# Kernel tuning notes

Hardware: AMD Instinct MI355X
Metric: run time of the kernel (lower is better)

Reference implementation:

```python
import jax, jax.numpy as jnp
import numpy as np
import math

B, T, C = 2, 2048, 1024
H, DK, DV = 16, 64, 64


def setup_inputs() -> dict:
    key = jax.random.key(0)
    ks = jax.random.split(key, 5)
    # randw(*d) = randn(*d) / sqrt(d[-1])
    x = jax.random.normal(ks[0], (B, T, C), dtype=jnp.float32)
    w_q = jax.random.normal(ks[1], (H, DK, C), dtype=jnp.float32) / math.sqrt(C)
    w_k = jax.random.normal(ks[2], (H, DK, C), dtype=jnp.float32) / math.sqrt(C)
    w_v = jax.random.normal(ks[3], (H, DV, C), dtype=jnp.float32) / math.sqrt(C)
    w_o = jax.random.normal(ks[4], (H * DV, C), dtype=jnp.float32) / math.sqrt(C)
    return {"x": x, "w_q": w_q, "w_k": w_k, "w_v": w_v, "w_o": w_o}


def reference(x, w_q, w_k, w_v, w_o):
    # Full prefill: bs_q.first = 0, bs_q.nb = T, causal=True, dropout=0 (eval).
    dk = w_q.shape[1]
    q = jnp.einsum('ntc,hdc->nhtd', x, w_q)  # [B,H,T,DK]
    k = jnp.einsum('ntc,hdc->nhtd', x, w_k)  # [B,H,T,DK]
    v = jnp.einsum('ntc,hdc->nhtd', x, w_v)  # [B,H,T,DV]
    a = jnp.einsum('nhtd,nhsd->nhts', q, k) / jnp.sqrt(jnp.asarray(dk, x.dtype))
    # amm_generator: mask where query_idx < key_idx (strict upper triangle)
    t = a.shape[-1]
    mask = jnp.arange(t)[:, None] < jnp.arange(t)[None, :]  # [T,T] bool
    a = jnp.where(mask[None, None], jnp.asarray(-jnp.inf, a.dtype), a)
    a = jax.nn.softmax(a, axis=-1)
    y = jnp.einsum('nhts,nhsd->nthd', a, v)  # [B,T,H,DV]
    y = y.reshape(y.shape[0], y.shape[1], -1)  # [B,T,H*DV]
    return y @ w_o  # [B,T,C]
```

## Files before the change

### kernel.cpp

```cpp
#include <hip/hip_runtime.h>
#include <hip/hip_bf16.h>

#define B_ 2
#define T_ 2048
#define C_ 1024
#define H_ 16
#define D_ 64

typedef __attribute__((ext_vector_type(8))) short bf16x8;
typedef __attribute__((ext_vector_type(4))) float f32x4;
typedef __attribute__((ext_vector_type(8))) unsigned short u16x8;
typedef __attribute__((ext_vector_type(2))) unsigned int u32x2;
typedef __attribute__((ext_vector_type(4))) unsigned int u32x4;

__device__ __forceinline__ unsigned short bf1(float a) {
    __bf16 x = (__bf16)a;
    return __builtin_bit_cast(unsigned short, x);
}
__device__ __forceinline__ unsigned int pk2(float a, float b) {
    return (unsigned int)bf1(a) | ((unsigned int)bf1(b) << 16);
}
__device__ __forceinline__ float bf2f(unsigned short u) {
    union { unsigned int u; float f; } v; v.u = (unsigned int)u << 16;
    return v.f;
}

__device__ __forceinline__ void gll16(const void* g, void* l) {
    __builtin_amdgcn_global_load_lds(
        (const __attribute__((address_space(1))) unsigned int*)g,
        (__attribute__((address_space(3))) unsigned int*)l, 16, 0, 0);
}

__global__ __launch_bounds__(256) void prep_x(
    const float* __restrict__ x, unsigned short* __restrict__ xb)
{
    const size_t i = ((size_t)blockIdx.x * 256 + threadIdx.x) * 16;
    float4 f0 = *reinterpret_cast<const float4*>(x + i);
    float4 f1 = *reinterpret_cast<const float4*>(x + i + 4);
    float4 f2 = *reinterpret_cast<const float4*>(x + i + 8);
    float4 f3 = *reinterpret_cast<const float4*>(x + i + 12);
    u32x4 a = {pk2(f0.x, f0.y), pk2(f0.z, f0.w), pk2(f1.x, f1.y), pk2(f1.z, f1.w)};
    u32x4 b = {pk2(f2.x, f2.y), pk2(f2.z, f2.w), pk2(f3.x, f3.y), pk2(f3.z, f3.w)};
    *reinterpret_cast<u32x4*>(xb + i) = a;
    *reinterpret_cast<u32x4*>(xb + i + 8) = b;
}

__global__ __launch_bounds__(256) void prep_w(
    const float* __restrict__ wq, const float* __restrict__ wk,
    const float* __restrict__ wv, unsigned short* __restrict__ wb)
{
    const int bid = blockIdx.x, tid = threadIdx.x;
    const int rb = bid * 4;
    const float* src = (rb < 1024) ? wq + (size_t)rb * 1024
                     : (rb < 2048) ? wk + (size_t)(rb - 1024) * 1024
                                   : wv + (size_t)(rb - 2048) * 1024;
    const float sc = (rb < 1024) ? 0.125f * 1.4426950408889634f : 1.0f;
    const float4* s4 = (const float4*)src;
    u32x2* d = (u32x2*)(wb + (size_t)rb * 1024);
#pragma unroll
    for (int k = 0; k < 4; k++) {
        float4 v = s4[k * 256 + tid];
        u32x2 w;
        w[0] = pk2(v.x * sc, v.y * sc);
        w[1] = pk2(v.z * sc, v.w * sc);
        d[k * 256 + tid] = w;
    }
}

__global__ __launch_bounds__(256) void prep_wo(
    const float* __restrict__ wo, unsigned short* __restrict__ wt)
{
    __shared__ unsigned short tile[64][72];
    const int tk = (blockIdx.x & 15) << 6, tn = (blockIdx.x >> 4) << 6;
    const int r = threadIdx.x >> 2, cb = (threadIdx.x & 3) << 4;
#pragma unroll
    for (int j = 0; j < 4; j++) {
        float4 v = *reinterpret_cast<const float4*>(
            wo + (size_t)(tk + r) * 1024 + tn + cb + j * 4);
        u32x2 w;
        w[0] = pk2(v.x, v.y);
        w[1] = pk2(v.z, v.w);
        *reinterpret_cast<u32x2*>(&tile[r][cb + j * 4]) = w;
    }
    __syncthreads();
    unsigned short buf[16];
#pragma unroll
    for (int j = 0; j < 16; j++) buf[j] = tile[cb + j][r];
    unsigned short* dst = wt + (size_t)(tn + r) * 1024 + tk + cb;
    *reinterpret_cast<u16x8*>(dst) = *reinterpret_cast<u16x8*>(buf);
    *reinterpret_cast<u16x8*>(dst + 8) = *reinterpret_cast<u16x8*>(buf + 8);
}

__global__ __launch_bounds__(256) void qkv_gemm(
    const unsigned short* __restrict__ xb, const unsigned short* __restrict__ wb,
    unsigned short* __restrict__ qkv)
{
    __shared__ __align__(16) unsigned short As[128 * 32];
    __shared__ __align__(16) unsigned short Bs[128 * 32];
    const int tid = threadIdx.x;
    const int lane = tid & 63, wave = tid >> 6;
    const int g = lane >> 4, c16 = lane & 15;
    const int xcd = blockIdx.x & 7, idx = blockIdx.x >> 3;
    const int bm = (xcd << 2) + idx / 24, bn = idx % 24;
    const int jbase = bn << 7;
    const int which = jbase >> 10;

    const int srow = lane >> 2, sch = (lane & 3) << 3;
    const unsigned short* asrc = xb + ((size_t)(bm << 7) + wave * 32 + srow) * C_ + sch;
    const unsigned short* bsrc = wb + ((size_t)(bn << 7) + wave * 32 + srow) * C_ + sch;

    f32x4 acc[4][4];
#pragma unroll
    for (int i = 0; i < 4; i++)
#pragma unroll
        for (int j = 0; j < 4; j++) acc[i][j] = (f32x4){0.f, 0.f, 0.f, 0.f};

    const int wm = (wave >> 1) << 6, wn = (wave & 1) << 6;

    for (int t = 0; t < 32; ++t) {
        const int k0 = t << 5;
        __syncthreads();
        gll16(asrc + k0,           &As[(wave * 32) << 5]);
        gll16(asrc + k0 + 16 * C_, &As[(wave * 32 + 16) << 5]);
        gll16(bsrc + k0,           &Bs[(wave * 32) << 5]);
        gll16(bsrc + k0 + 16 * C_, &Bs[(wave * 32 + 16) << 5]);
        __syncthreads();

        bf16x8 af[4], bfv[4];
#pragma unroll
        for (int m = 0; m < 4; m++)
            af[m] = *reinterpret_cast<const bf16x8*>(&As[((wm + m * 16 + c16) << 5) + g * 8]);
#pragma unroll
        for (int n = 0; n < 4; n++)
            bfv[n] = *reinterpret_cast<const bf16x8*>(&Bs[((wn + n * 16 + c16) << 5) + g * 8]);
#pragma unroll
        for (int m = 0; m < 4; m++)
#pragma unroll
            for (int n = 0; n < 4; n++)
                acc[m][n] = __builtin_amdgcn_mfma_f32_16x16x32_bf16(af[m], bfv[n], acc[m][n], 0, 0, 0);
    }

    if (which < 2) {
#pragma unroll
        for (int m = 0; m < 4; m++) {
            const int grow = (bm << 7) + wm + m * 16 + (g << 2);
#pragma unroll
            for (int n = 0; n < 4; n++) {
                const int jj = (jbase + wn + n * 16 + c16) & 1023;
                const int h = jj >> 6, d = jj & 63;
#pragma unroll
                for (int r = 0; r < 4; r++) {
                    const int row = grow + r;
                    const int b = row >> 11, t = row & 2047;
                    const size_t off = ((size_t)((which * B_ + b) * H_ + h) * T_ + t) * 64 + d;
                    qkv[off] = bf1(acc[m][n][r]);
                }
            }
        }
    } else {
#pragma unroll
        for (int m = 0; m < 4; m++) {
            const int grow = (bm << 7) + wm + m * 16 + (g << 2);
            const int b = grow >> 11, t = grow & 2047;
#pragma unroll
            for (int n = 0; n < 4; n++) {
                const int jj = (jbase + wn + n * 16 + c16) & 1023;
                const int h = jj >> 6, d = jj & 63;
                u32x2 w;
                w[0] = pk2(acc[m][n][0], acc[m][n][1]);
                w[1] = pk2(acc[m][n][2], acc[m][n][3]);
                const size_t off = ((size_t)((2 * B_ + b) * H_ + h) * 64 + d) * T_ + t;
                *reinterpret_cast<u32x2*>(&qkv[off]) = w;
            }
        }
    }
}

__global__ __launch_bounds__(256) void attn(
    const unsigned short* __restrict__ qkv,
    unsigned short* __restrict__ opA, unsigned short* __restrict__ opB,
    float* __restrict__ lbuf)
{
    __shared__ __align__(16) unsigned short Ks[2][64 * 64];
    __shared__ __align__(16) unsigned short Vt[2][64 * 64];
    __shared__ __align__(16) unsigned short Ps[4][16 * 64];
    const int tid = threadIdx.x, lane = tid & 63, wave = tid >> 6;
    const int g = lane >> 4, c16 = lane & 15;
    const int qt = 31 - (blockIdx.x >> 6);
    const int rem = blockIdx.x & 63;
    const int half = rem >> 5, bh = rem & 31;
    const int b = bh >> 4, h = bh & 15;
    const size_t headoff = (size_t)(b * H_ + h) * T_ * 64;
    const size_t QSZ = (size_t)B_ * H_ * T_ * 64;
    const unsigned short* qp = qkv + headoff;
    const unsigned short* kp = qkv + QSZ + headoff;
    const unsigned short* vTp = qkv + 2 * QSZ + headoff;

    const int nt = qt + 1;
    const int h1 = (nt + 1) >> 1;
    const int itlo = half ? h1 : 0, ithi = half ? nt : h1;

    const int qbase = (qt << 6) + wave * 16;
    bf16x8 qf0, qf1;
    {
        const size_t r0 = (size_t)(qbase + c16) * 64;
        qf0 = *reinterpret_cast<const bf16x8*>(qp + r0 + g * 8);
        qf1 = *reinterpret_cast<const bf16x8*>(qp + r0 + 32 + g * 8);
    }

    const bf16x8 ones = {0x3F80, 0x3F80, 0x3F80, 0x3F80, 0x3F80, 0x3F80, 0x3F80, 0x3F80};
    f32x4 lacc = (f32x4){0.f, 0.f, 0.f, 0.f};
    f32x4 acc[4];
#pragma unroll
    for (int i = 0; i < 4; i++) acc[i] = (f32x4){0.f, 0.f, 0.f, 0.f};

    const int srow8 = lane >> 3;
    const int swc = ((lane & 7) ^ srow8) << 3;
    const unsigned short* ksrc = kp + (size_t)(wave * 16 + srow8) * 64 + swc;
    const unsigned short* vsrc = vTp + (size_t)(wave * 16 + srow8) * T_ + swc;

    auto stage = [&](int buf, int s0) {
#pragma unroll
        for (int i = 0; i < 2; i++) {
            gll16(ksrc + (size_t)(s0 + i * 8) * 64, &Ks[buf][(wave * 16 + i * 8) << 6]);
            gll16(vsrc + s0 + (size_t)i * 8 * T_, &Vt[buf][(wave * 16 + i * 8) << 6]);
        }
    };

    if (itlo < ithi) {
        stage(0, itlo << 6);
        int cur = 0;
        for (int it = itlo; it < ithi; ++it) {
            __syncthreads();
            if (it + 1 < ithi) stage(cur ^ 1, (it + 1) << 6);
            const int s0 = it << 6;

            f32x4 sfT[4];
#pragma unroll
            for (int f = 0; f < 4; f++) sfT[f] = (f32x4){-16.f, -16.f, -16.f, -16.f};
            __builtin_amdgcn_s_setprio(1);
#pragma unroll
            for (int f = 0; f < 4; f++) {
                const int row = f * 16 + c16;
                const int sw = row & 7;
                bf16x8 k0 = *reinterpret_cast<const bf16x8*>(&Ks[cur][(row << 6) + ((g ^ sw) << 3)]);
                bf16x8 k1 = *reinterpret_cast<const bf16x8*>(&Ks[cur][(row << 6) + (((g + 4) ^ sw) << 3)]);
                sfT[f] = __builtin_amdgcn_mfma_f32_16x16x32_bf16(k0, qf0, sfT[f], 0, 0, 0);
                sfT[f] = __builtin_amdgcn_mfma_f32_16x16x32_bf16(k1, qf1, sfT[f], 0, 0, 0);
            }
            __builtin_amdgcn_s_setprio(0);

            if (it == qt) {
                const int qglob = qbase + c16;
#pragma unroll
                for (int f = 0; f < 4; f++)
#pragma unroll
                    for (int r = 0; r < 4; r++) {
                        const int kv = s0 + f * 16 + g * 4 + r;
                        if (kv > qglob) sfT[f][r] = -1e30f;
                    }
            }

#pragma unroll
            for (int f = 0; f < 4; f++)
#pragma unroll
                for (int r = 0; r < 4; r++)
                    sfT[f][r] = __builtin_amdgcn_exp2f(sfT[f][r]);

#pragma unroll
            for (int f = 0; f < 4; f++) {
                u32x2 w;
                w[0] = pk2(sfT[f][0], sfT[f][1]);
                w[1] = pk2(sfT[f][2], sfT[f][3]);
                const int addr = (c16 << 6) + ((((f << 1) + (g >> 1)) ^ (c16 & 7)) << 3) + ((g & 1) << 2);
                *reinterpret_cast<u32x2*>(&Ps[wave][addr]) = w;
            }

            __builtin_amdgcn_s_setprio(1);
#pragma unroll
            for (int ks = 0; ks < 2; ks++) {
                bf16x8 pa = *reinterpret_cast<const bf16x8*>(
                    &Ps[wave][(c16 << 6) + ((((ks << 2) + g) ^ (c16 & 7)) << 3)]);
                lacc = __builtin_amdgcn_mfma_f32_16x16x32_bf16(ones, pa, lacc, 0, 0, 0);
#pragma unroll
                for (int fd = 0; fd < 4; fd++) {
                    const int d = fd * 16 + c16;
                    bf16x8 vf = *reinterpret_cast<const bf16x8*>(
                        &Vt[cur][(d << 6) + ((((ks << 2) + g) ^ (d & 7)) << 3)]);
                    acc[fd] = __builtin_amdgcn_mfma_f32_16x16x32_bf16(vf, pa, acc[fd], 0, 0, 0);
                }
            }
            __builtin_amdgcn_s_setprio(0);
            cur ^= 1;
        }
    }

    unsigned short* op = half ? opB : opA;
#pragma unroll
    for (int fd = 0; fd < 4; fd++) {
        u32x2 w;
        w[0] = pk2(acc[fd][0], acc[fd][1]);
        w[1] = pk2(acc[fd][2], acc[fd][3]);
        const size_t cy = ((size_t)b * T_ + qbase + c16) * 1024 + h * 64 + fd * 16 + g * 4;
        *reinterpret_cast<u32x2*>(&op[cy]) = w;
    }
    if (lane < 16)
        lbuf[(size_t)half * (B_ * H_ * T_) + ((size_t)(b * H_ + h)) * T_ + qbase + c16] = lacc[0];
}

__global__ __launch_bounds__(256) void combine(
    const unsigned short* __restrict__ opA, const unsigned short* __restrict__ opB,
    const float* __restrict__ lbuf, unsigned short* __restrict__ y)
{
    const size_t i = ((size_t)blockIdx.x * 256 + threadIdx.x) * 8;
    const int hh = (int)((i >> 6) & 15);
    const int t = (int)((i >> 10) & 2047);
    const int bb = (int)(i >> 21);
    const size_t li = ((size_t)(bb * H_ + hh)) * T_ + t;
    const float inv = 1.0f / (lbuf[li] + lbuf[(size_t)B_ * H_ * T_ + li]);
    u16x8 a = *reinterpret_cast<const u16x8*>(opA + i);
    u16x8 c = *reinterpret_cast<const u16x8*>(opB + i);
    unsigned short o[8];
#pragma unroll
    for (int j = 0; j < 8; j++) o[j] = bf1((bf2f(a[j]) + bf2f(c[j])) * inv);
    *reinterpret_cast<u16x8*>(y + i) = *reinterpret_cast<u16x8*>(o);
}

__global__ __launch_bounds__(256) void out_proj(
    const unsigned short* __restrict__ y, const unsigned short* __restrict__ wt,
    float* __restrict__ out)
{
    __shared__ __align__(16) unsigned short As[128 * 32];
    __shared__ __align__(16) unsigned short Bs[64 * 32];
    const int tid = threadIdx.x;
    const int lane = tid & 63, wave = tid >> 6;
    const int g = lane >> 4, c16 = lane & 15;
    const int xcd = blockIdx.x & 7, idx = blockIdx.x >> 3;
    const int bm = (xcd << 2) + (idx >> 4), bn = idx & 15;
    const int wm = (wave >> 1) << 6, wn = (wave & 1) << 5;

    const int srow = lane >> 2, sch = (lane & 3) << 3;
    const unsigned short* ysrc = y + ((size_t)(bm << 7) + wave * 32 + srow) * 1024 + sch;
    const unsigned short* wsrc = wt + ((size_t)(bn << 6) + wave * 16 + srow) * 1024 + sch;

    f32x4 acc[4][2];
#pragma unroll
    for (int i = 0; i < 4; i++)
#pragma unroll
        for (int j = 0; j < 2; j++) acc[i][j] = (f32x4){0.f, 0.f, 0.f, 0.f};

    for (int t = 0; t < 32; ++t) {
        const int k0 = t << 5;
        __syncthreads();
        gll16(ysrc + k0,            &As[(wave * 32) << 5]);
        gll16(ysrc + k0 + 16 * 1024, &As[(wave * 32 + 16) << 5]);
        gll16(wsrc + k0,            &Bs[(wave * 16) << 5]);
        __syncthreads();

        bf16x8 af[4], bfr[2];
#pragma unroll
        for (int m = 0; m < 4; m++)
            af[m] = *reinterpret_cast<const bf16x8*>(&As[((wm + m * 16 + c16) << 5) + g * 8]);
#pragma unroll
        for (int n = 0; n < 2; n++)
            bfr[n] = *reinterpret_cast<const bf16x8*>(&Bs[((wn + n * 16 + c16) << 5) + g * 8]);
#pragma unroll
        for (int m = 0; m < 4; m++)
#pragma unroll
            for (int n = 0; n < 2; n++)
                acc[m][n] = __builtin_amdgcn_mfma_f32_16x16x32_bf16(af[m], bfr[n], acc[m][n], 0, 0, 0);
    }

#pragma unroll
    for (int m = 0; m < 4; m++) {
        const int grow = (bm << 7) + wm + m * 16 + (g << 2);
#pragma unroll
        for (int n = 0; n < 2; n++) {
            const int gcol = (bn << 6) + wn + n * 16 + c16;
#pragma unroll
            for (int r = 0; r < 4; r++)
                out[(size_t)(grow + r) * 1024 + gcol] = acc[m][n][r];
        }
    }
}

extern "C" void kernel_launch(void* const* d_in, const int* in_sizes, int n_in,
                              void* d_out, int out_size, void* d_ws, size_t ws_size,
                              hipStream_t stream) {
    const float* x  = (const float*)d_in[0];
    const float* wq = (const float*)d_in[1];
    const float* wk = (const float*)d_in[2];
    const float* wv = (const float*)d_in[3];
    const float* wo = (const float*)d_in[4];
    float* out = (float*)d_out;

    unsigned short* wb   = (unsigned short*)d_ws;
    unsigned short* opB  = (unsigned short*)d_ws;
    unsigned short* y    = opB;
    unsigned short* qkv  = (unsigned short*)d_ws + (size_t)4 * 1024 * 1024;
    unsigned short* wt   = qkv;
    unsigned short* xb   = (unsigned short*)d_out;
    unsigned short* opA  = (unsigned short*)d_out;
    float* lbuf = (float*)((char*)d_out + (size_t)8 * 1024 * 1024);

    prep_x<<<dim3(1024), 256, 0, stream>>>(x, xb);
    prep_w<<<dim3(768), 256, 0, stream>>>(wq, wk, wv, wb);
    qkv_gemm<<<dim3(768), 256, 0, stream>>>(xb, wb, qkv);
    attn<<<dim3(2048), 256, 0, stream>>>(qkv, opA, opB, lbuf);
    combine<<<dim3(4096), 256, 0, stream>>>(opA, opB, lbuf, y);
    prep_wo<<<dim3(256), 256, 0, stream>>>(wo, wt);
    out_proj<<<dim3(512), 256, 0, stream>>>(y, wt, out);
}
```

Measured before the change: 116.8 us.

## Process two query tiles per attention block to reuse staged K/V

Each attention block now handles 128 query rows (two 64-row tiles per wave set) instead of 64, so every K/V tile staged into shared memory feeds twice as many MFMAs. The KV range is split into two halves aligned to the 128-row tile, and the double-buffered loop is manually unrolled by two with precomputed swizzled LDS pointers. A fully masked first sub-tile skips its exp and PV work. This halves the grid and the global K/V traffic per query row, at the cost of more registers and fewer blocks to balance the causal workload.

New measurement: 116.7 us. Within noise of the previous version (-0.1%).

```diff
diff --git a/kernel.cpp b/kernel.cpp
--- a/kernel.cpp
+++ b/kernel.cpp
@@ -181,14 +181,14 @@
     unsigned short* __restrict__ opA, unsigned short* __restrict__ opB,
     float* __restrict__ lbuf)
 {
-    __shared__ __align__(16) unsigned short Ks[2][64 * 64];
-    __shared__ __align__(16) unsigned short Vt[2][64 * 64];
+    __shared__ __align__(16) unsigned short Ks0[64 * 64], Ks1[64 * 64];
+    __shared__ __align__(16) unsigned short Vt0[64 * 64], Vt1[64 * 64];
     __shared__ __align__(16) unsigned short Ps[4][16 * 64];
     const int tid = threadIdx.x, lane = tid & 63, wave = tid >> 6;
     const int g = lane >> 4, c16 = lane & 15;
-    const int qt = 31 - (blockIdx.x >> 6);
+    const int qt = 15 - (blockIdx.x >> 6);
     const int rem = blockIdx.x & 63;
-    const int half = rem >> 5, bh = rem & 31;
+    const int split = rem >> 5, bh = rem & 31;
     const int b = bh >> 4, h = bh & 15;
     const size_t headoff = (size_t)(b * H_ + h) * T_ * 64;
     const size_t QSZ = (size_t)B_ * H_ * T_ * 64;
@@ -196,116 +196,192 @@
     const unsigned short* kp = qkv + QSZ + headoff;
     const unsigned short* vTp = qkv + 2 * QSZ + headoff;
 
-    const int nt = qt + 1;
-    const int h1 = (nt + 1) >> 1;
-    const int itlo = half ? h1 : 0, ithi = half ? nt : h1;
-
-    const int qbase = (qt << 6) + wave * 16;
-    bf16x8 qf0, qf1;
+    const int h1 = qt + 1;
+    const int itlo = split ? h1 : 0, ithi = split ? (2 * qt + 2) : h1;
+
+    const int qb0 = (qt << 7) + wave * 16;
+    const int qb1 = qb0 + 64;
+    bf16x8 qf00, qf01, qf10, qf11;
     {
-        const size_t r0 = (size_t)(qbase + c16) * 64;
-        qf0 = *reinterpret_cast<const bf16x8*>(qp + r0 + g * 8);
-        qf1 = *reinterpret_cast<const bf16x8*>(qp + r0 + 32 + g * 8);
+        const size_t r0 = (size_t)(qb0 + c16) * 64;
+        const size_t r1 = (size_t)(qb1 + c16) * 64;
+        qf00 = *reinterpret_cast<const bf16x8*>(qp + r0 + g * 8);
+        qf01 = *reinterpret_cast<const bf16x8*>(qp + r0 + 32 + g * 8);
+        qf10 = *reinterpret_cast<const bf16x8*>(qp + r1 + g * 8);
+        qf11 = *reinterpret_cast<const bf16x8*>(qp + r1 + 32 + g * 8);
     }
 
     const bf16x8 ones = {0x3F80, 0x3F80, 0x3F80, 0x3F80, 0x3F80, 0x3F80, 0x3F80, 0x3F80};
-    f32x4 lacc = (f32x4){0.f, 0.f, 0.f, 0.f};
-    f32x4 acc[4];
-#pragma unroll
-    for (int i = 0; i < 4; i++) acc[i] = (f32x4){0.f, 0.f, 0.f, 0.f};
+    f32x4 lac0 = (f32x4){0.f, 0.f, 0.f, 0.f}, lac1 = (f32x4){0.f, 0.f, 0.f, 0.f};
+    f32x4 acc0[4], acc1[4];
+#pragma unroll
+    for (int i = 0; i < 4; i++) {
+        acc0[i] = (f32x4){0.f, 0.f, 0.f, 0.f};
+        acc1[i] = (f32x4){0.f, 0.f, 0.f, 0.f};
+    }
+
+    const int sw = c16 & 7;
+    const int rdo0 = (c16 << 6) + ((g ^ sw) << 3);
+    const int rdo1 = (c16 << 6) + (((g + 4) ^ sw) << 3);
+    const unsigned short* krA0 = Ks0 + rdo0;
+    const unsigned short* krA1 = Ks0 + rdo1;
+    const unsigned short* krB0 = Ks1 + rdo0;
+    const unsigned short* krB1 = Ks1 + rdo1;
+    const unsigned short* vrA0 = Vt0 + rdo0;
+    const unsigned short* vrA1 = Vt0 + rdo1;
+    const unsigned short* vrB0 = Vt1 + rdo0;
+    const unsigned short* vrB1 = Vt1 + rdo1;
+    const unsigned short* par0 = Ps[wave] + rdo0;
+    const unsigned short* par1 = Ps[wave] + rdo1;
+    unsigned short* pw[4];
+#pragma unroll
+    for (int f = 0; f < 4; f++)
+        pw[f] = Ps[wave] + (c16 << 6)
+              + (((((f << 1) + (g >> 1))) ^ sw) << 3) + ((g & 1) << 2);
 
     const int srow8 = lane >> 3;
     const int swc = ((lane & 7) ^ srow8) << 3;
     const unsigned short* ksrc = kp + (size_t)(wave * 16 + srow8) * 64 + swc;
     const unsigned short* vsrc = vTp + (size_t)(wave * 16 + srow8) * T_ + swc;
 
-    auto stage = [&](int buf, int s0) {
+    auto stageTo = [&](unsigned short* kd, unsigned short* vd, int s0) {
 #pragma unroll
         for (int i = 0; i < 2; i++) {
-            gll16(ksrc + (size_t)(s0 + i * 8) * 64, &Ks[buf][(wave * 16 + i * 8) << 6]);
-            gll16(vsrc + s0 + (size_t)i * 8 * T_, &Vt[buf][(wave * 16 + i * 8) << 6]);
+            gll16(ksrc + (size_t)(s0 + i * 8) * 64, kd + ((wave * 16 + i * 8) << 6));
+            gll16(vsrc + s0 + (size_t)i * 8 * T_, vd + ((wave * 16 + i * 8) << 6));
         }
     };
 
-    if (itlo < ithi) {
-        stage(0, itlo << 6);
-        int cur = 0;
-        for (int it = itlo; it < ithi; ++it) {
-            __syncthreads();
-            if (it + 1 < ithi) stage(cur ^ 1, (it + 1) << 6);
-            const int s0 = it << 6;
-
-            f32x4 sfT[4];
-#pragma unroll
-            for (int f = 0; f < 4; f++) sfT[f] = (f32x4){-16.f, -16.f, -16.f, -16.f};
-            __builtin_amdgcn_s_setprio(1);
-#pragma unroll
-            for (int f = 0; f < 4; f++) {
-                const int row = f * 16 + c16;
-                const int sw = row & 7;
-                bf16x8 k0 = *reinterpret_cast<const bf16x8*>(&Ks[cur][(row << 6) + ((g ^ sw) << 3)]);
-                bf16x8 k1 = *reinterpret_cast<const bf16x8*>(&Ks[cur][(row << 6) + (((g + 4) ^ sw) << 3)]);
-                sfT[f] = __builtin_amdgcn_mfma_f32_16x16x32_bf16(k0, qf0, sfT[f], 0, 0, 0);
-                sfT[f] = __builtin_amdgcn_mfma_f32_16x16x32_bf16(k1, qf1, sfT[f], 0, 0, 0);
-            }
-            __builtin_amdgcn_s_setprio(0);
-
-            if (it == qt) {
-                const int qglob = qbase + c16;
-#pragma unroll
-                for (int f = 0; f < 4; f++)
-#pragma unroll
-                    for (int r = 0; r < 4; r++) {
-                        const int kv = s0 + f * 16 + g * 4 + r;
-                        if (kv > qglob) sfT[f][r] = -1e30f;
-                    }
-            }
-
+    auto body = [&](const unsigned short* kr0, const unsigned short* kr1,
+                    const unsigned short* vr0, const unsigned short* vr1, int s0) {
+        f32x4 s0f[4], s1f[4];
+#pragma unroll
+        for (int f = 0; f < 4; f++) {
+            s0f[f] = (f32x4){-16.f, -16.f, -16.f, -16.f};
+            s1f[f] = (f32x4){-16.f, -16.f, -16.f, -16.f};
+        }
+        __builtin_amdgcn_s_setprio(1);
+#pragma unroll
+        for (int f = 0; f < 4; f++) {
+            bf16x8 k0 = *reinterpret_cast<const bf16x8*>(kr0 + f * 1024);
+            bf16x8 k1 = *reinterpret_cast<const bf16x8*>(kr1 + f * 1024);
+            s0f[f] = __builtin_amdgcn_mfma_f32_16x16x32_bf16(k0, qf00, s0f[f], 0, 0, 0);
+            s1f[f] = __builtin_amdgcn_mfma_f32_16x16x32_bf16(k0, qf10, s1f[f], 0, 0, 0);
+            s0f[f] = __builtin_amdgcn_mfma_f32_16x16x32_bf16(k1, qf01, s0f[f], 0, 0, 0);
+            s1f[f] = __builtin_amdgcn_mfma_f32_16x16x32_bf16(k1, qf11, s1f[f], 0, 0, 0);
+        }
+        __builtin_amdgcn_s_setprio(0);
+
+        if (s0 + 63 > qb0) {
+            const int qg = qb0 + c16;
 #pragma unroll
             for (int f = 0; f < 4; f++)
 #pragma unroll
                 for (int r = 0; r < 4; r++)
-                    sfT[f][r] = __builtin_amdgcn_exp2f(sfT[f][r]);
-
+                    if (s0 + f * 16 + g * 4 + r > qg) s0f[f][r] = -1e30f;
+        }
+        if (s0 + 63 > qb1) {
+            const int qg = qb1 + c16;
+#pragma unroll
+            for (int f = 0; f < 4; f++)
+#pragma unroll
+                for (int r = 0; r < 4; r++)
+                    if (s0 + f * 16 + g * 4 + r > qg) s1f[f][r] = -1e30f;
+        }
+
+        if (s0 <= qb0 + 15) {
+#pragma unroll
+            for (int f = 0; f < 4; f++)
+#pragma unroll
+                for (int r = 0; r < 4; r++)
+                    s0f[f][r] = __builtin_amdgcn_exp2f(s0f[f][r]);
 #pragma unroll
             for (int f = 0; f < 4; f++) {
                 u32x2 w;
-                w[0] = pk2(sfT[f][0], sfT[f][1]);
-                w[1] = pk2(sfT[f][2], sfT[f][3]);
-                const int addr = (c16 << 6) + ((((f << 1) + (g >> 1)) ^ (c16 & 7)) << 3) + ((g & 1) << 2);
-                *reinterpret_cast<u32x2*>(&Ps[wave][addr]) = w;
-            }
-
+                w[0] = pk2(s0f[f][0], s0f[f][1]);
+                w[1] = pk2(s0f[f][2], s0f[f][3]);
+                *reinterpret_cast<u32x2*>(pw[f]) = w;
+            }
             __builtin_amdgcn_s_setprio(1);
 #pragma unroll
             for (int ks = 0; ks < 2; ks++) {
-                bf16x8 pa = *reinterpret_cast<const bf16x8*>(
-                    &Ps[wave][(c16 << 6) + ((((ks << 2) + g) ^ (c16 & 7)) << 3)]);
-                lacc = __builtin_amdgcn_mfma_f32_16x16x32_bf16(ones, pa, lacc, 0, 0, 0);
+                bf16x8 pa = *reinterpret_cast<const bf16x8*>(ks ? par1 : par0);
+                const unsigned short* vp = ks ? vr1 : vr0;
+                lac0 = __builtin_amdgcn_mfma_f32_16x16x32_bf16(ones, pa, lac0, 0, 0, 0);
 #pragma unroll
                 for (int fd = 0; fd < 4; fd++) {
-                    const int d = fd * 16 + c16;
-                    bf16x8 vf = *reinterpret_cast<const bf16x8*>(
-                        &Vt[cur][(d << 6) + ((((ks << 2) + g) ^ (d & 7)) << 3)]);
-                    acc[fd] = __builtin_amdgcn_mfma_f32_16x16x32_bf16(vf, pa, acc[fd], 0, 0, 0);
+                    bf16x8 vf = *reinterpret_cast<const bf16x8*>(vp + fd * 1024);
+                    acc0[fd] = __builtin_amdgcn_mfma_f32_16x16x32_bf16(vf, pa, acc0[fd], 0, 0, 0);
                 }
             }
             __builtin_amdgcn_s_setprio(0);
-            cur ^= 1;
-        }
-    }
-
-    unsigned short* op = half ? opB : opA;
+        }
+
+        {
+#pragma unroll
+            for (int f = 0; f < 4; f++)
+#pragma unroll
+                for (int r = 0; r < 4; r++)
+                    s1f[f][r] = __builtin_amdgcn_exp2f(s1f[f][r]);
+#pragma unroll
+            for (int f = 0; f < 4; f++) {
+                u32x2 w;
+                w[0] = pk2(s1f[f][0], s1f[f][1]);
+                w[1] = pk2(s1f[f][2], s1f[f][3]);
+                *reinterpret_cast<u32x2*>(pw[f]) = w;
+            }
+            __builtin_amdgcn_s_setprio(1);
+#pragma unroll
+            for (int ks = 0; ks < 2; ks++) {
+                bf16x8 pa = *reinterpret_cast<const bf16x8*>(ks ? par1 : par0);
+                const unsigned short* vp = ks ? vr1 : vr0;
+                lac1 = __builtin_amdgcn_mfma_f32_16x16x32_bf16(ones, pa, lac1, 0, 0, 0);
+#pragma unroll
+                for (int fd = 0; fd < 4; fd++) {
+                    bf16x8 vf = *reinterpret_cast<const bf16x8*>(vp + fd * 1024);
+                    acc1[fd] = __builtin_amdgcn_mfma_f32_16x16x32_bf16(vf, pa, acc1[fd], 0, 0, 0);
+                }
+            }
+            __builtin_amdgcn_s_setprio(0);
+        }
+    };
+
+    if (itlo < ithi) {
+        stageTo(Ks0, Vt0, itlo << 6);
+        int it = itlo;
+        while (it + 2 <= ithi) {
+            __syncthreads();
+            stageTo(Ks1, Vt1, (it + 1) << 6);
+            body(krA0, krA1, vrA0, vrA1, it << 6);
+            __syncthreads();
+            if (it + 2 < ithi) stageTo(Ks0, Vt0, (it + 2) << 6);
+            body(krB0, krB1, vrB0, vrB1, (it + 1) << 6);
+            it += 2;
+        }
+        if (it < ithi) {
+            __syncthreads();
+            body(krA0, krA1, vrA0, vrA1, it << 6);
+        }
+    }
+
+    unsigned short* op = split ? opB : opA;
 #pragma unroll
     for (int fd = 0; fd < 4; fd++) {
-        u32x2 w;
-        w[0] = pk2(acc[fd][0], acc[fd][1]);
-        w[1] = pk2(acc[fd][2], acc[fd][3]);
-        const size_t cy = ((size_t)b * T_ + qbase + c16) * 1024 + h * 64 + fd * 16 + g * 4;
-        *reinterpret_cast<u32x2*>(&op[cy]) = w;
-    }
-    if (lane < 16)
-        lbuf[(size_t)half * (B_ * H_ * T_) + ((size_t)(b * H_ + h)) * T_ + qbase + c16] = lacc[0];
+        u32x2 w0, w1;
+        w0[0] = pk2(acc0[fd][0], acc0[fd][1]);
+        w0[1] = pk2(acc0[fd][2], acc0[fd][3]);
+        w1[0] = pk2(acc1[fd][0], acc1[fd][1]);
+        w1[1] = pk2(acc1[fd][2], acc1[fd][3]);
+        const size_t c0 = ((size_t)b * T_ + qb0 + c16) * 1024 + h * 64 + fd * 16 + g * 4;
+        const size_t c1 = ((size_t)b * T_ + qb1 + c16) * 1024 + h * 64 + fd * 16 + g * 4;
+        *reinterpret_cast<u32x2*>(&op[c0]) = w0;
+        *reinterpret_cast<u32x2*>(&op[c1]) = w1;
+    }
+    if (lane < 16) {
+        const size_t base = (size_t)split * (B_ * H_ * T_) + ((size_t)(b * H_ + h)) * T_;
+        lbuf[base + qb0 + c16] = lac0[0];
+        lbuf[base + qb1 + c16] = lac1[0];
+    }
 }
 
 __global__ __launch_bounds__(256) void combine(
@@ -406,7 +482,7 @@
     prep_x<<<dim3(1024), 256, 0, stream>>>(x, xb);
     prep_w<<<dim3(768), 256, 0, stream>>>(wq, wk, wv, wb);
     qkv_gemm<<<dim3(768), 256, 0, stream>>>(xb, wb, qkv);
-    attn<<<dim3(2048), 256, 0, stream>>>(qkv, opA, opB, lbuf);
+    attn<<<dim3(1024), 256, 0, stream>>>(qkv, opA, opB, lbuf);
     combine<<<dim3(4096), 256, 0, stream>>>(opA, opB, lbuf, y);
     prep_wo<<<dim3(256), 256, 0, stream>>>(wo, wt);
     out_proj<<<dim3(512), 256, 0, stream>>>(y, wt, out);
```
